# Kernel optimization log

Hardware: AMD Instinct MI355X
Metric: run time of the kernel (lower is better)

## Reference

```python
import jax, jax.numpy as jnp
from jax import lax
import numpy as np

LRELU_SLOPE = 0.1
DILATIONS = (1, 2, 4)
B, C, T = 8, 256, 8192


def pd_indexing(x, d, dilation):
    """Pitch-dependent past/future gather along time.
    x: (B, C, T); d: (B, 1, T) float dilation factors.
    Returns xP, xF: (B, C, T), zero where index is out of range.
    """
    b, c, t_len = x.shape
    t = jnp.arange(t_len, dtype=x.dtype)  # (T,)
    dil = d[:, 0, :] * dilation           # (B, T)
    idxP = jnp.round(t[None, :] - dil).astype(jnp.int32)  # (B, T)
    idxF = jnp.round(t[None, :] + dil).astype(jnp.int32)  # (B, T)
    validP = (idxP >= 0).astype(x.dtype)[:, None, :]        # (B,1,T)
    validF = (idxF < t_len).astype(x.dtype)[:, None, :]
    idxPc = jnp.broadcast_to(jnp.clip(idxP, 0, t_len - 1)[:, None, :], (b, c, t_len))
    idxFc = jnp.broadcast_to(jnp.clip(idxF, 0, t_len - 1)[:, None, :], (b, c, t_len))
    xP = jnp.take_along_axis(x, idxPc, axis=2) * validP
    xF = jnp.take_along_axis(x, idxFc, axis=2) * validF
    return xP, xF


def conv1x1(x, w, bias):
    # x: (B,C,T), w: (O,C), bias: (O,)
    return jnp.einsum('oc,bct->bot', w, x) + bias[None, :, None]


def conv3(x, w, bias):
    # x: (B,C,T), w: (O,C,3), padding=1
    y = lax.conv_general_dilated(x, w, window_strides=(1,), padding=[(1, 1)],
                                 dimension_numbers=('NCH', 'OIH', 'NCH'))
    return y + bias[None, :, None]


def setup_inputs() -> dict:
    key = jax.random.key(0)
    ks = jax.random.split(key, 8)
    x = jax.random.normal(ks[0], (B, C, T), dtype=jnp.float32)
    d = jax.random.uniform(ks[1], (B, 1, T), dtype=jnp.float32, minval=0.0, maxval=16.0)
    n = len(DILATIONS)
    s1 = 1.0 / np.sqrt(C)
    s3 = 1.0 / np.sqrt(3 * C)
    WC = jax.random.normal(ks[2], (n, C, C), dtype=jnp.float32) * s1
    WP = jax.random.normal(ks[3], (n, C, C), dtype=jnp.float32) * s1
    WF = jax.random.normal(ks[4], (n, C, C), dtype=jnp.float32) * s1
    WA = jax.random.normal(ks[5], (n, C, C, 3), dtype=jnp.float32) * s3
    bC = jnp.zeros((n, C), dtype=jnp.float32)
    bP = jnp.zeros((n, C), dtype=jnp.float32)
    bF = jnp.zeros((n, C), dtype=jnp.float32)
    bA = jnp.zeros((n, C), dtype=jnp.float32)
    return {"x": x, "d": d, "WC": WC, "bC": bC, "WP": WP, "bP": bP,
            "WF": WF, "bF": bF, "WA": WA, "bA": bA}


def reference(x, d, WC, bC, WP, bP, WF, bF, WA, bA):
    for i, dilation in enumerate(DILATIONS):
        xt = jax.nn.leaky_relu(x, LRELU_SLOPE)
        xP, xF = pd_indexing(xt, d, dilation)
        xt = conv1x1(xt, WC[i], bC[i]) + conv1x1(xP, WP[i], bP[i]) + conv1x1(xF, WF[i], bF[i])
        xt = jax.nn.leaky_relu(xt, LRELU_SLOPE)
        xt = conv3(xt, WA[i], bA[i])
        x = xt + x
    return x
```

## Files before the change

### kernel.cpp

```cpp
#include <hip/hip_runtime.h>
#include <hip/hip_bf16.h>
#include <cstddef>
#include <cstdint>

constexpr int Bn = 8, Cn = 256, Tn = 8192;
constexpr int NL = 3;
constexpr int Kc = 768;
constexpr float SLOPE = 0.1f;

typedef unsigned short u16;
using bf8   = __attribute__((ext_vector_type(8))) short;
using f32x4 = __attribute__((ext_vector_type(4))) float;

__device__ __forceinline__ float lrelu(float v) { return v > 0.f ? v : SLOPE * v; }
__device__ __forceinline__ u16 f2bf(float f) {
    __hip_bfloat16 h = __float2bfloat16(f);
    return *reinterpret_cast<u16*>(&h);
}

__global__ __launch_bounds__(256)
void k_wprep(const float* __restrict__ WC, const float* __restrict__ WP,
             const float* __restrict__ WF, const float* __restrict__ WA,
             const float* __restrict__ bC, const float* __restrict__ bP,
             const float* __restrict__ bF,
             u16* __restrict__ Wcat, u16* __restrict__ WAp, float* __restrict__ bSum)
{
    const int n1 = NL * Cn * Kc;
    for (int i = blockIdx.x * blockDim.x + threadIdx.x; i < n1;
         i += gridDim.x * blockDim.x) {
        int c = i % Cn;
        int s = (i / Cn) % 3;
        int o = (i / (3 * Cn)) % Cn;
        int l = i / (3 * Cn * Cn);
        size_t src = ((size_t)l * Cn + o) * Cn + c;
        float wc = (s == 0) ? WC[src] : (s == 1) ? WP[src] : WF[src];
        Wcat[i] = f2bf(wc);
        WAp[i] = f2bf(WA[src * 3 + s]);
    }
    for (int i = blockIdx.x * blockDim.x + threadIdx.x; i < NL * Cn;
         i += gridDim.x * blockDim.x)
        bSum[i] = bC[i] + bP[i] + bF[i];
}

__global__ __launch_bounds__(256)
void k_prep(const float* __restrict__ x, u16* __restrict__ xT)
{
    __shared__ float s[64][65];
    const int b = blockIdx.z, c0 = blockIdx.y * 64, t0 = blockIdx.x * 64;
    const int tid = threadIdx.x;
    const float* xb = x + ((size_t)b * Cn + c0) * Tn + t0;

    int tt = tid & 63, c4 = tid >> 6;
    for (int cc = c4; cc < 64; cc += 4)
        s[cc][tt] = xb[(size_t)cc * Tn + tt];
    __syncthreads();

    int ccS = tid & 63, t4 = tid >> 6;
    u16* xTb = xT + ((size_t)b * Tn + t0) * Cn + c0;
    for (int t2 = t4; t2 < 64; t2 += 4)
        xTb[(size_t)t2 * Cn + ccS] = f2bf(lrelu(s[ccS][t2]));
}

__global__ __launch_bounds__(256)
void k_gemm1(const u16* __restrict__ xT, const float* __restrict__ d,
             const u16* __restrict__ Wl, const float* __restrict__ bS,
             float dil, u16* __restrict__ zT)
{
    __shared__ u16 sX[128 * 32];
    __shared__ u16 sW[128 * 32];
    __shared__ int sRow[3][128];

    const int tid = threadIdx.x;
    const int b = blockIdx.z;
    const int t0 = blockIdx.x * 128;
    const int o0 = blockIdx.y * 128;

    if (tid < 128) {
        int t = t0 + tid;
        float dv = d[(size_t)b * Tn + t] * dil;
        int ip = (int)rintf((float)t - dv);
        int iF = (int)rintf((float)t + dv);
        sRow[0][tid] = t;
        sRow[1][tid] = (ip >= 0) ? ip : -1;
        sRow[2][tid] = (iF < Tn) ? iF : -1;
    }
    __syncthreads();

    const int srow = tid >> 2;
    const int schunk = (tid & 3) * 8;
    int rA0[3], rA1[3];
    #pragma unroll
    for (int s = 0; s < 3; ++s) { rA0[s] = sRow[s][srow]; rA1[s] = sRow[s][srow + 64]; }

    const int lane = tid & 63, wv = tid >> 6;
    const int wm = (wv & 1) * 64;
    const int wn = (wv >> 1) * 64;
    const int lr = lane & 15, quad = lane >> 4;

    f32x4 acc[4][4] = {};
    const u16* xTb = xT + (size_t)b * Tn * Cn;

    for (int kg = 0; kg < Kc; kg += 32) {
        const int seg = kg >> 8, c0 = kg & 255;
        const u16* wsrc = Wl + (size_t)(o0 + srow) * Kc + kg + schunk;
        uint4 w0 = *(const uint4*)wsrc;
        uint4 w1 = *(const uint4*)(wsrc + (size_t)64 * Kc);
        uint4 x0 = {0, 0, 0, 0}, x1 = {0, 0, 0, 0};
        int r0 = rA0[seg], r1 = rA1[seg];
        if (r0 >= 0) x0 = *(const uint4*)(xTb + (size_t)r0 * Cn + c0 + schunk);
        if (r1 >= 0) x1 = *(const uint4*)(xTb + (size_t)r1 * Cn + c0 + schunk);
        __syncthreads();
        *(uint4*)(sW + srow * 32 + schunk) = w0;
        *(uint4*)(sW + (srow + 64) * 32 + schunk) = w1;
        *(uint4*)(sX + srow * 32 + schunk) = x0;
        *(uint4*)(sX + (srow + 64) * 32 + schunk) = x1;
        __syncthreads();

        bf8 af[4], bg[4];
        #pragma unroll
        for (int mi = 0; mi < 4; ++mi)
            af[mi] = *(const bf8*)(sX + (wm + mi * 16 + lr) * 32 + quad * 8);
        #pragma unroll
        for (int ni = 0; ni < 4; ++ni)
            bg[ni] = *(const bf8*)(sW + (wn + ni * 16 + lr) * 32 + quad * 8);
        #pragma unroll
        for (int mi = 0; mi < 4; ++mi)
            #pragma unroll
            for (int ni = 0; ni < 4; ++ni)
                acc[mi][ni] = __builtin_amdgcn_mfma_f32_16x16x32_bf16(
                    af[mi], bg[ni], acc[mi][ni], 0, 0, 0);
    }

    float bias[4];
    #pragma unroll
    for (int ni = 0; ni < 4; ++ni) bias[ni] = bS[o0 + wn + ni * 16 + lr];
    u16* zTb = zT + (size_t)b * Tn * Cn;
    #pragma unroll
    for (int mi = 0; mi < 4; ++mi)
        #pragma unroll
        for (int r = 0; r < 4; ++r) {
            int t = t0 + wm + mi * 16 + quad * 4 + r;
            u16* row = zTb + (size_t)t * Cn + o0 + wn;
            #pragma unroll
            for (int ni = 0; ni < 4; ++ni)
                row[ni * 16 + lr] = f2bf(lrelu(acc[mi][ni][r] + bias[ni]));
        }
}

__global__ __launch_bounds__(256)
void k_gemm2(const u16* __restrict__ zT, const u16* __restrict__ WAl,
             const float* __restrict__ bA, const float* __restrict__ xres,
             float* __restrict__ out)
{
    __shared__ u16 sZ[128 * 32];
    __shared__ u16 sW[128 * 32];

    const int tid = threadIdx.x;
    const int b = blockIdx.z;
    const int t0 = blockIdx.x * 128;
    const int o0 = blockIdx.y * 128;

    const int srow = tid >> 2;
    const int schunk = (tid & 3) * 8;
    const int lane = tid & 63, wv = tid >> 6;
    const int wo = (wv & 1) * 64;
    const int wt = (wv >> 1) * 64;
    const int lr = lane & 15, quad = lane >> 4;

    f32x4 acc[4][4] = {};
    const u16* zTb = zT + (size_t)b * Tn * Cn;

    for (int kg = 0; kg < Kc; kg += 32) {
        const int tap = kg >> 8, c0 = kg & 255;
        const u16* wsrc = WAl + (size_t)(o0 + srow) * Kc + kg + schunk;
        uint4 w0 = *(const uint4*)wsrc;
        uint4 w1 = *(const uint4*)(wsrc + (size_t)64 * Kc);
        int r0 = t0 + srow + tap - 1;
        int r1 = r0 + 64;
        uint4 z0 = {0, 0, 0, 0}, z1 = {0, 0, 0, 0};
        if (r0 >= 0 && r0 < Tn) z0 = *(const uint4*)(zTb + (size_t)r0 * Cn + c0 + schunk);
        if (r1 >= 0 && r1 < Tn) z1 = *(const uint4*)(zTb + (size_t)r1 * Cn + c0 + schunk);
        __syncthreads();
        *(uint4*)(sW + srow * 32 + schunk) = w0;
        *(uint4*)(sW + (srow + 64) * 32 + schunk) = w1;
        *(uint4*)(sZ + srow * 32 + schunk) = z0;
        *(uint4*)(sZ + (srow + 64) * 32 + schunk) = z1;
        __syncthreads();

        bf8 af[4], bg[4];
        #pragma unroll
        for (int mi = 0; mi < 4; ++mi)
            af[mi] = *(const bf8*)(sW + (wo + mi * 16 + lr) * 32 + quad * 8);
        #pragma unroll
        for (int ni = 0; ni < 4; ++ni)
            bg[ni] = *(const bf8*)(sZ + (wt + ni * 16 + lr) * 32 + quad * 8);
        #pragma unroll
        for (int mi = 0; mi < 4; ++mi)
            #pragma unroll
            for (int ni = 0; ni < 4; ++ni)
                acc[mi][ni] = __builtin_amdgcn_mfma_f32_16x16x32_bf16(
                    af[mi], bg[ni], acc[mi][ni], 0, 0, 0);
    }

    #pragma unroll
    for (int mi = 0; mi < 4; ++mi)
        #pragma unroll
        for (int r = 0; r < 4; ++r) {
            int o = o0 + wo + mi * 16 + quad * 4 + r;
            float bv = bA[o];
            size_t base = ((size_t)b * Cn + o) * Tn + t0 + wt;
            #pragma unroll
            for (int ni = 0; ni < 4; ++ni) {
                size_t idx = base + ni * 16 + lr;
                out[idx] = acc[mi][ni][r] + bv + xres[idx];
            }
        }
}

extern "C" void kernel_launch(void* const* d_in, const int* in_sizes, int n_in,
                              void* d_out, int out_size, void* d_ws, size_t ws_size,
                              hipStream_t stream)
{
    const float* x  = (const float*)d_in[0];
    const float* d  = (const float*)d_in[1];
    const float* WC = (const float*)d_in[2];
    const float* bC = (const float*)d_in[3];
    const float* WP = (const float*)d_in[4];
    const float* bP = (const float*)d_in[5];
    const float* WF = (const float*)d_in[6];
    const float* bF = (const float*)d_in[7];
    const float* WA = (const float*)d_in[8];
    const float* bA = (const float*)d_in[9];
    float* out = (float*)d_out;

    char* ws = (char*)d_ws;
    u16*   xT   = (u16*)(ws);
    u16*   zT   = (u16*)(ws + (size_t)Bn * Tn * Cn * 2);
    u16*   Wcat = (u16*)(ws + (size_t)2 * Bn * Tn * Cn * 2);
    u16*   WAp  = Wcat + (size_t)NL * Cn * Kc;
    float* bSum = (float*)(WAp + (size_t)NL * Cn * Kc);

    k_wprep<<<dim3(1024), dim3(256), 0, stream>>>(WC, WP, WF, WA, bC, bP, bF,
                                                  Wcat, WAp, bSum);

    dim3 gP(Tn / 64, Cn / 64, Bn);
    dim3 gG(Tn / 128, Cn / 128, Bn);
    dim3 blk(256);

    const float dils[NL] = {1.f, 2.f, 4.f};
    const float* xcur = x;
    for (int i = 0; i < NL; ++i) {
        k_prep<<<gP, blk, 0, stream>>>(xcur, xT);
        k_gemm1<<<gG, blk, 0, stream>>>(xT, d,
                                        Wcat + (size_t)i * Cn * Kc,
                                        bSum + (size_t)i * Cn,
                                        dils[i], zT);
        k_gemm2<<<gG, blk, 0, stream>>>(zT,
                                        WAp + (size_t)i * Cn * Kc,
                                        bA + (size_t)i * Cn,
                                        xcur, out);
        xcur = out;
    }
}
```

Measured before the change: 438.5 us.

## Use direct global-to-LDS loads and fuse next-layer transpose into gemm2 epilogue

Both GEMM kernels now stage tiles with global_load_lds instead of going through registers. A shared zero row replaces the branches for out-of-range gathers. The gemm2 epilogue also writes the leaky-ReLU bf16 transposed activations for the next layer through an LDS strip, which removes two of the three k_prep launches and their extra read of the fp32 residual. In exchange, direct LDS loads bypass register staging, and the epilogue gains extra syncs and shared-memory traffic.

After: 418.3 us. 4.6% less time.

```diff
diff --git a/kernel.cpp b/kernel.cpp
--- a/kernel.cpp
+++ b/kernel.cpp
@@ -16,6 +16,12 @@
 __device__ __forceinline__ u16 f2bf(float f) {
     __hip_bfloat16 h = __float2bfloat16(f);
     return *reinterpret_cast<u16*>(&h);
+}
+
+__device__ __forceinline__ void g2l16(const u16* g, u16* l) {
+    __builtin_amdgcn_global_load_lds(
+        (const __attribute__((address_space(1))) char*)g,
+        (__attribute__((address_space(3))) char*)l, 16, 0, 0);
 }
 
 __global__ __launch_bounds__(256)
@@ -23,8 +29,10 @@
              const float* __restrict__ WF, const float* __restrict__ WA,
              const float* __restrict__ bC, const float* __restrict__ bP,
              const float* __restrict__ bF,
-             u16* __restrict__ Wcat, u16* __restrict__ WAp, float* __restrict__ bSum)
-{
+             u16* __restrict__ Wcat, u16* __restrict__ WAp, float* __restrict__ bSum,
+             u16* __restrict__ zrow)
+{
+    if (blockIdx.x == 0) zrow[threadIdx.x] = 0;
     const int n1 = NL * Cn * Kc;
     for (int i = blockIdx.x * blockDim.x + threadIdx.x; i < n1;
          i += gridDim.x * blockDim.x) {
@@ -64,7 +72,7 @@
 __global__ __launch_bounds__(256)
 void k_gemm1(const u16* __restrict__ xT, const float* __restrict__ d,
              const u16* __restrict__ Wl, const float* __restrict__ bS,
-             float dil, u16* __restrict__ zT)
+             float dil, u16* __restrict__ zT, const u16* __restrict__ zrow)
 {
     __shared__ u16 sX[128 * 32];
     __shared__ u16 sW[128 * 32];
@@ -88,9 +96,15 @@
 
     const int srow = tid >> 2;
     const int schunk = (tid & 3) * 8;
-    int rA0[3], rA1[3];
-    #pragma unroll
-    for (int s = 0; s < 3; ++s) { rA0[s] = sRow[s][srow]; rA1[s] = sRow[s][srow + 64]; }
+    const u16* xTb = xT + (size_t)b * Tn * Cn;
+
+    const u16 *pr0[3], *pr1[3];
+    #pragma unroll
+    for (int s = 0; s < 3; ++s) {
+        int r0 = sRow[s][srow], r1 = sRow[s][srow + 64];
+        pr0[s] = (r0 >= 0) ? (xTb + (size_t)r0 * Cn + schunk) : (zrow + schunk);
+        pr1[s] = (r1 >= 0) ? (xTb + (size_t)r1 * Cn + schunk) : (zrow + schunk);
+    }
 
     const int lane = tid & 63, wv = tid >> 6;
     const int wm = (wv & 1) * 64;
@@ -98,37 +112,36 @@
     const int lr = lane & 15, quad = lane >> 4;
 
     f32x4 acc[4][4] = {};
-    const u16* xTb = xT + (size_t)b * Tn * Cn;
-
-    for (int kg = 0; kg < Kc; kg += 32) {
-        const int seg = kg >> 8, c0 = kg & 255;
-        const u16* wsrc = Wl + (size_t)(o0 + srow) * Kc + kg + schunk;
-        uint4 w0 = *(const uint4*)wsrc;
-        uint4 w1 = *(const uint4*)(wsrc + (size_t)64 * Kc);
-        uint4 x0 = {0, 0, 0, 0}, x1 = {0, 0, 0, 0};
-        int r0 = rA0[seg], r1 = rA1[seg];
-        if (r0 >= 0) x0 = *(const uint4*)(xTb + (size_t)r0 * Cn + c0 + schunk);
-        if (r1 >= 0) x1 = *(const uint4*)(xTb + (size_t)r1 * Cn + c0 + schunk);
-        __syncthreads();
-        *(uint4*)(sW + srow * 32 + schunk) = w0;
-        *(uint4*)(sW + (srow + 64) * 32 + schunk) = w1;
-        *(uint4*)(sX + srow * 32 + schunk) = x0;
-        *(uint4*)(sX + (srow + 64) * 32 + schunk) = x1;
-        __syncthreads();
-
-        bf8 af[4], bg[4];
-        #pragma unroll
-        for (int mi = 0; mi < 4; ++mi)
-            af[mi] = *(const bf8*)(sX + (wm + mi * 16 + lr) * 32 + quad * 8);
-        #pragma unroll
-        for (int ni = 0; ni < 4; ++ni)
-            bg[ni] = *(const bf8*)(sW + (wn + ni * 16 + lr) * 32 + quad * 8);
-        #pragma unroll
-        for (int mi = 0; mi < 4; ++mi)
+
+    #pragma unroll
+    for (int seg = 0; seg < 3; ++seg) {
+        const u16* xr0 = pr0[seg];
+        const u16* xr1 = pr1[seg];
+        const u16* wp0 = Wl + (size_t)(o0 + srow) * Kc + seg * 256 + schunk;
+        const u16* wp1 = wp0 + (size_t)64 * Kc;
+        #pragma unroll
+        for (int kk = 0; kk < 256; kk += 32) {
+            __syncthreads();
+            g2l16(wp0 + kk, sW + srow * 32 + schunk);
+            g2l16(wp1 + kk, sW + (srow + 64) * 32 + schunk);
+            g2l16(xr0 + kk, sX + srow * 32 + schunk);
+            g2l16(xr1 + kk, sX + (srow + 64) * 32 + schunk);
+            __syncthreads();
+
+            bf8 af[4], bg[4];
+            #pragma unroll
+            for (int mi = 0; mi < 4; ++mi)
+                af[mi] = *(const bf8*)(sX + (wm + mi * 16 + lr) * 32 + quad * 8);
             #pragma unroll
             for (int ni = 0; ni < 4; ++ni)
-                acc[mi][ni] = __builtin_amdgcn_mfma_f32_16x16x32_bf16(
-                    af[mi], bg[ni], acc[mi][ni], 0, 0, 0);
+                bg[ni] = *(const bf8*)(sW + (wn + ni * 16 + lr) * 32 + quad * 8);
+            #pragma unroll
+            for (int mi = 0; mi < 4; ++mi)
+                #pragma unroll
+                for (int ni = 0; ni < 4; ++ni)
+                    acc[mi][ni] = __builtin_amdgcn_mfma_f32_16x16x32_bf16(
+                        af[mi], bg[ni], acc[mi][ni], 0, 0, 0);
+        }
     }
 
     float bias[4];
@@ -150,10 +163,12 @@
 __global__ __launch_bounds__(256)
 void k_gemm2(const u16* __restrict__ zT, const u16* __restrict__ WAl,
              const float* __restrict__ bA, const float* __restrict__ xres,
-             float* __restrict__ out)
-{
-    __shared__ u16 sZ[128 * 32];
-    __shared__ u16 sW[128 * 32];
+             float* __restrict__ out, u16* __restrict__ xTn, int writeXT,
+             const u16* __restrict__ zrow)
+{
+    __shared__ u16 smem[128 * 32 * 2];
+    u16* sZ = smem;
+    u16* sW = smem + 4096;
 
     const int tid = threadIdx.x;
     const int b = blockIdx.z;
@@ -170,51 +185,90 @@
     f32x4 acc[4][4] = {};
     const u16* zTb = zT + (size_t)b * Tn * Cn;
 
-    for (int kg = 0; kg < Kc; kg += 32) {
-        const int tap = kg >> 8, c0 = kg & 255;
-        const u16* wsrc = WAl + (size_t)(o0 + srow) * Kc + kg + schunk;
-        uint4 w0 = *(const uint4*)wsrc;
-        uint4 w1 = *(const uint4*)(wsrc + (size_t)64 * Kc);
-        int r0 = t0 + srow + tap - 1;
-        int r1 = r0 + 64;
-        uint4 z0 = {0, 0, 0, 0}, z1 = {0, 0, 0, 0};
-        if (r0 >= 0 && r0 < Tn) z0 = *(const uint4*)(zTb + (size_t)r0 * Cn + c0 + schunk);
-        if (r1 >= 0 && r1 < Tn) z1 = *(const uint4*)(zTb + (size_t)r1 * Cn + c0 + schunk);
-        __syncthreads();
-        *(uint4*)(sW + srow * 32 + schunk) = w0;
-        *(uint4*)(sW + (srow + 64) * 32 + schunk) = w1;
-        *(uint4*)(sZ + srow * 32 + schunk) = z0;
-        *(uint4*)(sZ + (srow + 64) * 32 + schunk) = z1;
-        __syncthreads();
-
-        bf8 af[4], bg[4];
-        #pragma unroll
-        for (int mi = 0; mi < 4; ++mi)
-            af[mi] = *(const bf8*)(sW + (wo + mi * 16 + lr) * 32 + quad * 8);
-        #pragma unroll
-        for (int ni = 0; ni < 4; ++ni)
-            bg[ni] = *(const bf8*)(sZ + (wt + ni * 16 + lr) * 32 + quad * 8);
-        #pragma unroll
-        for (int mi = 0; mi < 4; ++mi)
+    #pragma unroll
+    for (int tap = 0; tap < 3; ++tap) {
+        const int r0 = t0 + srow + tap - 1;
+        const int r1 = r0 + 64;
+        const u16* zr0 = (r0 >= 0 && r0 < Tn) ? (zTb + (size_t)r0 * Cn + schunk)
+                                              : (zrow + schunk);
+        const u16* zr1 = (r1 >= 0 && r1 < Tn) ? (zTb + (size_t)r1 * Cn + schunk)
+                                              : (zrow + schunk);
+        const u16* wp0 = WAl + (size_t)(o0 + srow) * Kc + tap * 256 + schunk;
+        const u16* wp1 = wp0 + (size_t)64 * Kc;
+        #pragma unroll
+        for (int kk = 0; kk < 256; kk += 32) {
+            __syncthreads();
+            g2l16(wp0 + kk, sW + srow * 32 + schunk);
+            g2l16(wp1 + kk, sW + (srow + 64) * 32 + schunk);
+            g2l16(zr0 + kk, sZ + srow * 32 + schunk);
+            g2l16(zr1 + kk, sZ + (srow + 64) * 32 + schunk);
+            __syncthreads();
+
+            bf8 af[4], bg[4];
+            #pragma unroll
+            for (int mi = 0; mi < 4; ++mi)
+                af[mi] = *(const bf8*)(sW + (wo + mi * 16 + lr) * 32 + quad * 8);
             #pragma unroll
             for (int ni = 0; ni < 4; ++ni)
-                acc[mi][ni] = __builtin_amdgcn_mfma_f32_16x16x32_bf16(
-                    af[mi], bg[ni], acc[mi][ni], 0, 0, 0);
-    }
-
-    #pragma unroll
-    for (int mi = 0; mi < 4; ++mi)
-        #pragma unroll
-        for (int r = 0; r < 4; ++r) {
-            int o = o0 + wo + mi * 16 + quad * 4 + r;
-            float bv = bA[o];
-            size_t base = ((size_t)b * Cn + o) * Tn + t0 + wt;
-            #pragma unroll
-            for (int ni = 0; ni < 4; ++ni) {
-                size_t idx = base + ni * 16 + lr;
-                out[idx] = acc[mi][ni][r] + bv + xres[idx];
+                bg[ni] = *(const bf8*)(sZ + (wt + ni * 16 + lr) * 32 + quad * 8);
+            #pragma unroll
+            for (int mi = 0; mi < 4; ++mi)
+                #pragma unroll
+                for (int ni = 0; ni < 4; ++ni)
+                    acc[mi][ni] = __builtin_amdgcn_mfma_f32_16x16x32_bf16(
+                        af[mi], bg[ni], acc[mi][ni], 0, 0, 0);
+        }
+    }
+
+    float biasv[4][4];
+    #pragma unroll
+    for (int mi = 0; mi < 4; ++mi) {
+        float4 bb = *(const float4*)(bA + o0 + wo + mi * 16 + quad * 4);
+        biasv[mi][0] = bb.x; biasv[mi][1] = bb.y; biasv[mi][2] = bb.z; biasv[mi][3] = bb.w;
+    }
+
+    if (writeXT) {
+        u16* strip = smem + wv * 1152;
+        u16* xTb2 = xTn + (size_t)b * Tn * Cn;
+        #pragma unroll
+        for (int ni = 0; ni < 4; ++ni) {
+            __syncthreads();
+            #pragma unroll
+            for (int mi = 0; mi < 4; ++mi) {
+                ushort4 pk;
+                #pragma unroll
+                for (int r = 0; r < 4; ++r) {
+                    int o = o0 + wo + mi * 16 + quad * 4 + r;
+                    size_t idx = ((size_t)b * Cn + o) * Tn + t0 + wt + ni * 16 + lr;
+                    float v = acc[mi][ni][r] + biasv[mi][r] + xres[idx];
+                    out[idx] = v;
+                    ((u16*)&pk)[r] = f2bf(lrelu(v));
+                }
+                *(ushort4*)(strip + lr * 72 + mi * 16 + quad * 4) = pk;
+            }
+            __syncthreads();
+            #pragma unroll
+            for (int it = 0; it < 2; ++it) {
+                int tt = (lane >> 3) + it * 8;
+                uint4 vv = *(const uint4*)(strip + tt * 72 + (lane & 7) * 8);
+                *(uint4*)(xTb2 + (size_t)(t0 + wt + ni * 16 + tt) * Cn
+                          + o0 + wo + (lane & 7) * 8) = vv;
             }
         }
+    } else {
+        #pragma unroll
+        for (int mi = 0; mi < 4; ++mi)
+            #pragma unroll
+            for (int r = 0; r < 4; ++r) {
+                int o = o0 + wo + mi * 16 + quad * 4 + r;
+                size_t base = ((size_t)b * Cn + o) * Tn + t0 + wt;
+                #pragma unroll
+                for (int ni = 0; ni < 4; ++ni) {
+                    size_t idx = base + ni * 16 + lr;
+                    out[idx] = acc[mi][ni][r] + biasv[mi][r] + xres[idx];
+                }
+            }
+    }
 }
 
 extern "C" void kernel_launch(void* const* d_in, const int* in_sizes, int n_in,
@@ -239,26 +293,29 @@
     u16*   Wcat = (u16*)(ws + (size_t)2 * Bn * Tn * Cn * 2);
     u16*   WAp  = Wcat + (size_t)NL * Cn * Kc;
     float* bSum = (float*)(WAp + (size_t)NL * Cn * Kc);
+    u16*   zrow = (u16*)(bSum + NL * Cn);
 
     k_wprep<<<dim3(1024), dim3(256), 0, stream>>>(WC, WP, WF, WA, bC, bP, bF,
-                                                  Wcat, WAp, bSum);
+                                                  Wcat, WAp, bSum, zrow);
 
     dim3 gP(Tn / 64, Cn / 64, Bn);
     dim3 gG(Tn / 128, Cn / 128, Bn);
     dim3 blk(256);
 
+    k_prep<<<gP, blk, 0, stream>>>(x, xT);
+
     const float dils[NL] = {1.f, 2.f, 4.f};
     const float* xcur = x;
     for (int i = 0; i < NL; ++i) {
-        k_prep<<<gP, blk, 0, stream>>>(xcur, xT);
         k_gemm1<<<gG, blk, 0, stream>>>(xT, d,
                                         Wcat + (size_t)i * Cn * Kc,
                                         bSum + (size_t)i * Cn,
-                                        dils[i], zT);
+                                        dils[i], zT, zrow);
         k_gemm2<<<gG, blk, 0, stream>>>(zT,
                                         WAp + (size_t)i * Cn * Kc,
                                         bA + (size_t)i * Cn,
-                                        xcur, out);
+                                        xcur, out, xT, (i < NL - 1) ? 1 : 0,
+                                        zrow);
         xcur = out;
     }
 }
```
